# Performance work log

Hardware: AMD Instinct MI355X
Metric: run time of the kernel (lower is better)

The kernel has to match this reference:

```python
import jax, jax.numpy as jnp
import numpy as np

N, E, G = 150000, 600000, 5000
NI, EI, GF, H, C = 16, 8, 32, 64, 40


def setup_inputs() -> dict:
    key = jax.random.key(0)
    ks = jax.random.split(key, 20)
    s = lambda fan: 1.0 / np.sqrt(fan)
    return {
        "x": jax.random.normal(ks[0], (N, NI), jnp.float32),
        "edge_index": jax.random.randint(ks[1], (2, E), 0, N),
        "edge_attr": jax.random.normal(ks[2], (E, EI), jnp.float32),
        "batch": jnp.sort(jax.random.randint(ks[3], (N,), 0, G)),
        "pocket_features": jax.random.normal(ks[4], (G, GF), jnp.float32),
        # edge MLP: Linear(EI,H) -> ReLU -> Linear(H, H*NI)
        "W_e1": jax.random.normal(ks[5], (EI, H), jnp.float32) * s(EI),
        "b_e1": jnp.zeros((H,), jnp.float32),
        "W_e2": jax.random.normal(ks[6], (H, H * NI), jnp.float32) * s(H),
        "b_e2": jnp.zeros((H * NI,), jnp.float32),
        # NNConv root weight + bias
        "root": jax.random.normal(ks[7], (NI, H), jnp.float32) * s(NI),
        "conv_bias": jnp.zeros((H,), jnp.float32),
        # GlobalAttention gate Linear(H,1)
        "Wg": jax.random.normal(ks[8], (H, 1), jnp.float32) * s(H),
        "bg": jnp.zeros((1,), jnp.float32),
        # fc1: input is concat [h_node(H), global_ctx(H), pocket(GF)]
        "W_fc1": jax.random.normal(ks[9], (2 * H + GF, H), jnp.float32) * s(2 * H + GF),
        "b_fc1": jnp.zeros((H,), jnp.float32),
        "W_np": jax.random.normal(ks[10], (H, C), jnp.float32) * s(H),
        "b_np": jnp.zeros((C,), jnp.float32),
        "W_sp": jax.random.normal(ks[11], (H, 1), jnp.float32) * s(H),
        "b_sp": jnp.zeros((1,), jnp.float32),
    }


def reference(x, edge_index, edge_attr, batch, pocket_features,
              W_e1, b_e1, W_e2, b_e2, root, conv_bias, Wg, bg,
              W_fc1, b_fc1, W_np, b_np, W_sp, b_sp):
    n, ni = x.shape
    h = root.shape[1]
    g = pocket_features.shape[0]
    src, dst = edge_index[0], edge_index[1]

    # NNConv: edge MLP -> per-edge weight matrix [E, NI, H]
    eh = jax.nn.relu(edge_attr @ W_e1 + b_e1)
    We = (eh @ W_e2 + b_e2).reshape(-1, ni, h)
    msg = jnp.einsum('ei,eih->eh', x[src], We)          # per-edge matmul
    agg = jax.ops.segment_sum(msg, dst, num_segments=n)
    cnt = jax.ops.segment_sum(jnp.ones(msg.shape[0], x.dtype), dst, num_segments=n)
    agg = agg / jnp.maximum(cnt, 1.0)[:, None]          # aggr='mean'
    h_node = jax.nn.relu(agg + x @ root + conv_bias)    # [N, H]

    # GlobalAttention pooling: scatter-softmax over nodes per graph
    gate = (h_node @ Wg + bg).squeeze(-1)               # [N]
    m = jax.ops.segment_max(gate, batch, num_segments=g)
    e = jnp.exp(gate - m[batch])
    denom = jax.ops.segment_sum(e, batch, num_segments=g)
    attn = e / denom[batch]
    gctx = jax.ops.segment_sum(attn[:, None] * h_node, batch, num_segments=g)
    gc = gctx[batch]                                    # broadcast back [N, H]

    feat = jnp.concatenate([h_node, gc, pocket_features[batch]], axis=1)
    f = jax.nn.relu(feat @ W_fc1 + b_fc1)
    node_pred = jax.nn.log_softmax(f @ W_np + b_np, axis=-1)
    stop = jax.nn.sigmoid((gc @ W_sp + b_sp).squeeze(-1))
    return node_pred, stop
```

## Files before the change

kernel.cpp:

```cpp
#include <hip/hip_runtime.h>
#include <hip/hip_bf16.h>
#include <math.h>

#define NN 150000
#define EE 600000
#define GG 5000
#define NI 16
#define EI 8
#define GFD 32
#define HH 64
#define CC 40

#define W2SZ (68 * 1024)
#define FPAD 68
#define NBLK ((NN + 1023) / 1024)

typedef __attribute__((ext_vector_type(8))) short short8v;
typedef __attribute__((ext_vector_type(16))) float f32x16;
typedef __attribute__((ext_vector_type(2))) float f32x2;

__device__ __forceinline__ unsigned short f2bf(float f) {
    __hip_bfloat16 h = __float2bfloat16(f);
    return __builtin_bit_cast(unsigned short, h);
}
__device__ __forceinline__ float bf2f(unsigned short u) {
    return __uint_as_float(((unsigned)u) << 16);
}
__device__ __forceinline__ unsigned cvtpk(float lo, float hi) {
    unsigned r;
    asm("v_cvt_pk_bf16_f32 %0, %1, %2" : "=v"(r) : "v"(lo), "v"(hi));
    return r;
}
__device__ __forceinline__ f32x2 pkmul(f32x2 a, f32x2 b) {
    f32x2 p;
    asm("v_pk_mul_f32 %0, %1, %2" : "=v"(p) : "v"(a), "v"(b));
    return p;
}
__device__ __forceinline__ short8v zfrag(float eh, const f32x2 (&xs2)[4]) {
    f32x2 ehp; ehp[0] = eh; ehp[1] = eh;
    union { short8v v; unsigned u[4]; } A;
    #pragma unroll
    for (int q = 0; q < 4; ++q) {
        f32x2 p = pkmul(ehp, xs2[q]);
        A.u[q] = cvtpk(p[0], p[1]);
    }
    return A.v;
}
__device__ __forceinline__ short8v xfrag(const f32x2 (&xs2)[4]) {
    union { short8v v; unsigned u[4]; } A;
    #pragma unroll
    for (int q = 0; q < 4; ++q)
        A.u[q] = cvtpk(xs2[q][0], xs2[q][1]);
    return A.v;
}

__global__ void k0_prep(const float* __restrict__ W_e2, const float* __restrict__ b_e2,
                        const float* __restrict__ W_fc1, const float* __restrict__ W_np,
                        const float* __restrict__ W_e1,
                        unsigned short* __restrict__ W2c,
                        unsigned short* __restrict__ W1aT,
                        unsigned short* __restrict__ W_npT,
                        unsigned short* __restrict__ W1e,
                        int* __restrict__ cursor)
{
    int idx = blockIdx.x * 256 + threadIdx.x;
    if (idx < W2SZ) {
        int c = idx >> 10, rem = idx & 1023;
        int r = rem >> 4, kk = rem & 15;
        float v = 0.f;
        if (c < 64)       v = W_e2[c * 1024 + kk * 64 + r];
        else if (c == 64) v = b_e2[kk * 64 + r];
        W2c[idx] = f2bf(v);
    } else if (idx < W2SZ + 4096) {
        int i = idx - W2SZ;
        int h = i >> 6, k = i & 63;
        W1aT[i] = f2bf(W_fc1[k * 64 + h]);
    } else if (idx < W2SZ + 8192) {
        int i = idx - W2SZ - 4096;
        int c = i >> 6, h = i & 63;
        W_npT[i] = f2bf(c < CC ? W_np[h * CC + c] : 0.f);
    } else if (idx < W2SZ + 8704) {
        int i = idx - W2SZ - 8192;
        int col = i >> 3, q = i & 7;
        W1e[i] = f2bf(W_e1[q * 64 + col]);
    } else if (idx < W2SZ + 8704 + NN) {
        cursor[idx - W2SZ - 8704] = 0;
    }
}

__global__ void kE_local(const int* __restrict__ ei, int* __restrict__ cursor,
                         int* __restrict__ rank)
{
    int e = blockIdx.x * 256 + threadIdx.x;
    if (e < EE) rank[e] = atomicAdd(&cursor[ei[EE + e]], 1);
}

__global__ void kB_scan1(const int* __restrict__ cnt, int* __restrict__ base,
                         int* __restrict__ bsum)
{
    __shared__ int sS[256];
    int b = blockIdx.x, t = threadIdx.x;
    int i0 = b * 1024 + t * 4;
    int v0 = (i0 + 0 < NN) ? cnt[i0 + 0] : 0;
    int v1 = (i0 + 1 < NN) ? cnt[i0 + 1] : 0;
    int v2 = (i0 + 2 < NN) ? cnt[i0 + 2] : 0;
    int v3 = (i0 + 3 < NN) ? cnt[i0 + 3] : 0;
    int tot = v0 + v1 + v2 + v3;
    sS[t] = tot;
    __syncthreads();
    int acc = tot;
    for (int off = 1; off < 256; off <<= 1) {
        int xv = (t >= off) ? sS[t - off] : 0;
        __syncthreads();
        acc += xv;
        sS[t] = acc;
        __syncthreads();
    }
    int run = acc - tot;
    if (i0 + 0 < NN) base[i0 + 0] = run; run += v0;
    if (i0 + 1 < NN) base[i0 + 1] = run; run += v1;
    if (i0 + 2 < NN) base[i0 + 2] = run; run += v2;
    if (i0 + 3 < NN) base[i0 + 3] = run;
    if (t == 255) bsum[b] = acc;
}

__global__ void kC_scan2(int* __restrict__ bsum)
{
    __shared__ int sS[256];
    int t = threadIdx.x;
    int v = (t < NBLK) ? bsum[t] : 0;
    sS[t] = v;
    __syncthreads();
    int acc = v;
    for (int off = 1; off < 256; off <<= 1) {
        int xv = (t >= off) ? sS[t - off] : 0;
        __syncthreads();
        acc += xv;
        sS[t] = acc;
        __syncthreads();
    }
    if (t < NBLK) bsum[t] = acc - v;
}

__device__ __forceinline__ void mfma_step(
    const unsigned short (&sEHT)[65][256], int c, int pf,
    const unsigned short* __restrict__ Bq0, const unsigned short* __restrict__ Bq1,
    int mb, int mr, const f32x2 (&xs0)[4], const f32x2 (&xs1)[4],
    short8v& curb0, short8v& curb1,
    f32x16& acc00, f32x16& acc01, f32x16& acc10, f32x16& acc11)
{
    short8v n0 = *(const short8v*)(Bq0 + pf * 1024);
    short8v n1 = *(const short8v*)(Bq1 + pf * 1024);
    int cc = (c & 31) << 1;
    float eh0 = bf2f(sEHT[c][(mb + mr) ^ cc]);
    float eh1 = bf2f(sEHT[c][(mb + 32 + mr) ^ cc]);
    short8v a0 = zfrag(eh0, xs0);
    short8v a1 = zfrag(eh1, xs1);
    __builtin_amdgcn_s_setprio(1);
    acc00 = __builtin_amdgcn_mfma_f32_32x32x16_bf16(a0, curb0, acc00, 0, 0, 0);
    acc01 = __builtin_amdgcn_mfma_f32_32x32x16_bf16(a0, curb1, acc01, 0, 0, 0);
    acc10 = __builtin_amdgcn_mfma_f32_32x32x16_bf16(a1, curb0, acc10, 0, 0, 0);
    acc11 = __builtin_amdgcn_mfma_f32_32x32x16_bf16(a1, curb1, acc11, 0, 0, 0);
    __builtin_amdgcn_s_setprio(0);
    curb0 = n0; curb1 = n1;
}

template<bool TWOPHASE>
__global__ __launch_bounds__(256, 4) void k1_mfma(
    const float* __restrict__ x, const int* __restrict__ ei,
    const float* __restrict__ ea,
    const unsigned short* __restrict__ W1e, const float* __restrict__ b_e1,
    const unsigned short* __restrict__ W2c,
    const int* __restrict__ rank, const int* __restrict__ base,
    const int* __restrict__ bsum,
    unsigned* __restrict__ msg16, float* __restrict__ agg)
{
    __shared__ unsigned short sEHT[65][256];
    __shared__ int sIdx[256];

    const int t = threadIdx.x;
    const long long eb = (long long)blockIdx.x * 256;

    const int lane = t & 63;
    const int w = t >> 6;
    const int mr = lane & 31;
    const int half = lane >> 5;
    const int mb = w * 64;

    {
        long long ge = eb + t;
        if (ge < EE) {
            int d = ei[EE + ge];
            sIdx[t] = TWOPHASE ? (base[d] + bsum[d >> 10] + rank[ge]) : d;
        } else {
            sIdx[t] = -1;
        }
        sEHT[64][t] = (unsigned short)0x3F80;
    }

    {
        short8v bW0, bW1;
        if (half == 0) {
            bW0 = *(const short8v*)(W1e + (size_t)mr * 8);
            bW1 = *(const short8v*)(W1e + (size_t)(32 + mr) * 8);
        } else {
            #pragma unroll
            for (int q = 0; q < 8; ++q) { bW0[q] = 0; bW1[q] = 0; }
        }
        float bias0 = b_e1[mr];
        float bias1 = b_e1[32 + mr];
        #pragma unroll
        for (int m = 0; m < 2; ++m) {
            int e_loc = w * 64 + m * 32 + mr;
            long long ge = eb + e_loc;
            short8v a;
            if (half == 0 && ge < EE) {
                const float4* eap = (const float4*)(ea + ge * EI);
                float4 u0 = eap[0], u1 = eap[1];
                union { short8v v; unsigned u[4]; } A;
                A.u[0] = cvtpk(u0.x, u0.y); A.u[1] = cvtpk(u0.z, u0.w);
                A.u[2] = cvtpk(u1.x, u1.y); A.u[3] = cvtpk(u1.z, u1.w);
                a = A.v;
            } else {
                #pragma unroll
                for (int q = 0; q < 8; ++q) a[q] = 0;
            }
            #pragma unroll
            for (int n = 0; n < 2; ++n) {
                f32x16 c_;
                #pragma unroll
                for (int r = 0; r < 16; ++r) c_[r] = 0.f;
                c_ = __builtin_amdgcn_mfma_f32_32x32x16_bf16(a, n ? bW1 : bW0, c_, 0, 0, 0);
                int kcol = n * 32 + mr;
                float bias = n ? bias1 : bias0;
                #pragma unroll
                for (int r = 0; r < 16; r += 2) {
                    int row = (r & 3) + 8 * (r >> 2) + 4 * half;
                    int e0 = w * 64 + m * 32 + row;
                    float v0 = fmaxf(c_[r]     + bias, 0.f);
                    float v1 = fmaxf(c_[r + 1] + bias, 0.f);
                    *(unsigned*)&sEHT[kcol][e0 ^ (mr << 1)] = cvtpk(v0, v1);
                }
            }
        }
    }

    f32x2 xs0[4], xs1[4];
    {
        long long e0 = eb + mb + mr;
        long long e1 = eb + mb + 32 + mr;
        if (e0 < EE) {
            int s0 = ei[e0];
            const float4* xp = (const float4*)(x + (size_t)s0 * NI + half * 8);
            float4 u0 = xp[0], u1 = xp[1];
            xs0[0][0]=u0.x; xs0[0][1]=u0.y; xs0[1][0]=u0.z; xs0[1][1]=u0.w;
            xs0[2][0]=u1.x; xs0[2][1]=u1.y; xs0[3][0]=u1.z; xs0[3][1]=u1.w;
        } else {
            #pragma unroll
            for (int q = 0; q < 4; ++q) { xs0[q][0] = 0.f; xs0[q][1] = 0.f; }
        }
        if (e1 < EE) {
            int s1 = ei[e1];
            const float4* xp = (const float4*)(x + (size_t)s1 * NI + half * 8);
            float4 u0 = xp[0], u1 = xp[1];
            xs1[0][0]=u0.x; xs1[0][1]=u0.y; xs1[1][0]=u0.z; xs1[1][1]=u0.w;
            xs1[2][0]=u1.x; xs1[2][1]=u1.y; xs1[3][0]=u1.z; xs1[3][1]=u1.w;
        } else {
            #pragma unroll
            for (int q = 0; q < 4; ++q) { xs1[q][0] = 0.f; xs1[q][1] = 0.f; }
        }
    }
    __syncthreads();

    f32x16 acc00, acc01, acc10, acc11;
    #pragma unroll
    for (int r = 0; r < 16; ++r) { acc00[r] = 0.f; acc01[r] = 0.f; acc10[r] = 0.f; acc11[r] = 0.f; }

    const unsigned short* Bq0 = W2c + mr * 16 + half * 8;
    const unsigned short* Bq1 = Bq0 + 512;

    short8v bA0 = *(const short8v*)(Bq0);
    short8v bA1 = *(const short8v*)(Bq1);
    short8v bB0 = *(const short8v*)(Bq0 + 1024);
    short8v bB1 = *(const short8v*)(Bq1 + 1024);

    #pragma unroll 2
    for (int c = 0; c < 64; c += 2) {
        mfma_step(sEHT, c,     c + 2, Bq0, Bq1, mb, mr, xs0, xs1, bA0, bA1, acc00, acc01, acc10, acc11);
        mfma_step(sEHT, c + 1, c + 3, Bq0, Bq1, mb, mr, xs0, xs1, bB0, bB1, acc00, acc01, acc10, acc11);
    }
    {
        short8v a0 = xfrag(xs0);
        short8v a1 = xfrag(xs1);
        __builtin_amdgcn_s_setprio(1);
        acc00 = __builtin_amdgcn_mfma_f32_32x32x16_bf16(a0, bA0, acc00, 0, 0, 0);
        acc01 = __builtin_amdgcn_mfma_f32_32x32x16_bf16(a0, bA1, acc01, 0, 0, 0);
        acc10 = __builtin_amdgcn_mfma_f32_32x32x16_bf16(a1, bA0, acc10, 0, 0, 0);
        acc11 = __builtin_amdgcn_mfma_f32_32x32x16_bf16(a1, bA1, acc11, 0, 0, 0);
        __builtin_amdgcn_s_setprio(0);
    }

    #pragma unroll
    for (int r = 0; r < 16; ++r) {
        int row = (r & 3) + 8 * (r >> 2) + 4 * half;
        int i0 = sIdx[mb + row];
        int i1 = sIdx[mb + 32 + row];
        if (TWOPHASE) {
            if (i0 >= 0) msg16[(size_t)i0 * 32 + mr] = cvtpk(acc00[r], acc01[r]);
            if (i1 >= 0) msg16[(size_t)i1 * 32 + mr] = cvtpk(acc10[r], acc11[r]);
        } else {
            if (i0 >= 0) {
                atomicAdd(&agg[(size_t)i0 * 64 + mr],      acc00[r]);
                atomicAdd(&agg[(size_t)i0 * 64 + 32 + mr], acc01[r]);
            }
            if (i1 >= 0) {
                atomicAdd(&agg[(size_t)i1 * 64 + mr],      acc10[r]);
                atomicAdd(&agg[(size_t)i1 * 64 + 32 + mr], acc11[r]);
            }
        }
    }
}

__global__ __launch_bounds__(256) void k2_red(
    const unsigned* __restrict__ msg16, const int* __restrict__ base,
    const int* __restrict__ bsum,
    const float* __restrict__ x, const float* __restrict__ root,
    const float* __restrict__ conv_bias,
    unsigned short* __restrict__ hn16,
    const float* __restrict__ Wg, const float* __restrict__ bg,
    float* __restrict__ gate)
{
    __shared__ float sroot[16][64];
    int t = threadIdx.x;
    #pragma unroll
    for (int q = 0; q < 4; ++q) {
        int i = q * 256 + t;
        sroot[i >> 6][i & 63] = root[i];
    }
    __syncthreads();

    int n = blockIdx.x * 4 + (t >> 6);
    int l = t & 63;
    int mr = l & 31, so = l >> 5;
    int s = base[n] + bsum[n >> 10];
    int e = (n == NN - 1) ? EE : base[n + 1] + bsum[(n + 1) >> 10];

    float alo = 0.f, ahi = 0.f;
    for (int sl = s + so; sl < e; sl += 2) {
        unsigned u = msg16[(size_t)sl * 32 + mr];
        alo += __uint_as_float(u << 16);
        ahi += __uint_as_float(u & 0xFFFF0000u);
    }
    alo += __shfl_xor(alo, 32);
    ahi += __shfl_xor(ahi, 32);
    float acc = (l < 32) ? alo : ahi;

    float inv = 1.0f / fmaxf((float)(e - s), 1.0f);
    float v = acc * inv + conv_bias[l];
    float xv = (l < 16) ? x[(size_t)n * NI + l] : 0.f;
    #pragma unroll
    for (int i = 0; i < 16; ++i)
        v = fmaf(__shfl(xv, i), sroot[i][l], v);
    v = fmaxf(v, 0.f);
    hn16[(size_t)n * 64 + l] = f2bf(v);

    float gv = v * Wg[l];
    #pragma unroll
    for (int off = 32; off; off >>= 1) gv += __shfl_xor(gv, off);
    if (l == 0) gate[n] = gv + bg[0];
}

__global__ __launch_bounds__(256) void k2_node(
    const float* __restrict__ agg, const int* __restrict__ base,
    const int* __restrict__ bsum,
    const float* __restrict__ x, const float* __restrict__ root,
    const float* __restrict__ conv_bias,
    unsigned short* __restrict__ hn16,
    const float* __restrict__ Wg, const float* __restrict__ bg,
    float* __restrict__ gate)
{
    int t = threadIdx.x;
    int n = blockIdx.x * 4 + (t >> 6);
    int h = t & 63;
    int s = base[n] + bsum[n >> 10];
    int e = (n == NN - 1) ? EE : base[n + 1] + bsum[(n + 1) >> 10];
    float inv = 1.0f / fmaxf((float)(e - s), 1.0f);
    float v = agg[(size_t)n * 64 + h] * inv + conv_bias[h];
    const float* xp = x + (size_t)n * NI;
    #pragma unroll
    for (int i = 0; i < NI; ++i) v += xp[i] * root[i * 64 + h];
    v = fmaxf(v, 0.f);
    hn16[(size_t)n * 64 + h] = f2bf(v);
    float gv = v * Wg[h];
    #pragma unroll
    for (int off = 32; off; off >>= 1) gv += __shfl_xor(gv, off);
    if (h == 0) gate[n] = gv + bg[0];
}

__device__ __forceinline__ int lbound(const int* __restrict__ b, int v) {
    int lo = 0, hi = NN;
    while (lo < hi) { int mid = (lo + hi) >> 1; if (b[mid] < v) lo = mid + 1; else hi = mid; }
    return lo;
}

__global__ __launch_bounds__(64) void k3_pool(
    const float* __restrict__ gate, const int* __restrict__ batch,
    const unsigned short* __restrict__ hn16, const float* __restrict__ pocket,
    const float* __restrict__ W_fc1, const float* __restrict__ b_fc1,
    const float* __restrict__ W_sp, const float* __restrict__ b_sp,
    float* __restrict__ pg, float* __restrict__ sg)
{
    int g = blockIdx.x;
    int lane = threadIdx.x;
    int s = lbound(batch, g);
    int e = lbound(batch, g + 1);

    float gcv = 0.f;
    if (e > s) {
        float m = -INFINITY;
        for (int n = s + lane; n < e; n += 64) m = fmaxf(m, gate[n]);
        #pragma unroll
        for (int off = 32; off; off >>= 1) m = fmaxf(m, __shfl_xor(m, off));
        float acc = 0.f, den = 0.f;
        for (int n = s; n < e; ++n) {
            float ev = expf(gate[n] - m);
            den += ev;
            acc += ev * bf2f(hn16[(size_t)n * 64 + lane]);
        }
        gcv = acc / den;
    }

    float sv = gcv * W_sp[lane];
    #pragma unroll
    for (int off = 32; off; off >>= 1) sv += __shfl_xor(sv, off);
    if (lane == 0) sg[g] = 1.f / (1.f + expf(-(sv + b_sp[0])));

    float pk = (lane < GFD) ? pocket[(size_t)g * GFD + lane] : 0.f;
    float pgv = b_fc1[lane];
    #pragma unroll 8
    for (int kk = 0; kk < 64; ++kk)
        pgv = fmaf(__shfl(gcv, kk), W_fc1[(64 + kk) * 64 + lane], pgv);
    #pragma unroll 8
    for (int kk = 0; kk < 32; ++kk)
        pgv = fmaf(__shfl(pk, kk), W_fc1[(128 + kk) * 64 + lane], pgv);
    pg[(size_t)g * 64 + lane] = pgv;
}

__global__ __launch_bounds__(256, 4) void k4_mfma(
    const unsigned short* __restrict__ hn16, const int* __restrict__ batch,
    const float* __restrict__ pg, const float* __restrict__ sg,
    const unsigned short* __restrict__ W1aT, const unsigned short* __restrict__ W_npT,
    const float* __restrict__ b_np,
    float* __restrict__ out_np, float* __restrict__ out_stop)
{
    __shared__ __align__(16) float sF[4][32][FPAD];
    __shared__ int sB[128];

    const int t = threadIdx.x;
    const int wv = t >> 6, lane = t & 63;
    const int mr = lane & 31, half = lane >> 5;
    const int nb = blockIdx.x * 128;

    if (t < 128) {
        int n = nb + t;
        sB[t] = (n < NN) ? batch[n] : 0;
    }

    const int node = nb + wv * 32 + mr;

    f32x16 acc0, acc1;
    #pragma unroll
    for (int r = 0; r < 16; ++r) { acc0[r] = 0.f; acc1[r] = 0.f; }

    #pragma unroll
    for (int c = 0; c < 4; ++c) {
        short8v a;
        if (node < NN) {
            a = *(const short8v*)(hn16 + (size_t)node * 64 + c * 16 + half * 8);
        } else {
            #pragma unroll
            for (int q = 0; q < 8; ++q) a[q] = 0;
        }
        short8v b0 = *(const short8v*)(W1aT + (size_t)mr * 64        + c * 16 + half * 8);
        short8v b1 = *(const short8v*)(W1aT + (size_t)(mr + 32) * 64 + c * 16 + half * 8);
        acc0 = __builtin_amdgcn_mfma_f32_32x32x16_bf16(a, b0, acc0, 0, 0, 0);
        acc1 = __builtin_amdgcn_mfma_f32_32x32x16_bf16(a, b1, acc1, 0, 0, 0);
    }
    __syncthreads();

    #pragma unroll
    for (int r = 0; r < 16; ++r) {
        int row = (r & 3) + 8 * (r >> 2) + 4 * half;
        int g = sB[wv * 32 + row];
        float p0 = pg[(size_t)g * 64 + mr];
        float p1 = pg[(size_t)g * 64 + 32 + mr];
        sF[wv][row][mr]      = fmaxf(acc0[r] + p0, 0.f);
        sF[wv][row][32 + mr] = fmaxf(acc1[r] + p1, 0.f);
    }

    f32x16 acc2, acc3;
    #pragma unroll
    for (int r = 0; r < 16; ++r) { acc2[r] = 0.f; acc3[r] = 0.f; }

    #pragma unroll
    for (int c = 0; c < 4; ++c) {
        const float* fp = &sF[wv][mr][c * 16 + half * 8];
        float4 u0 = *(const float4*)(fp);
        float4 u1 = *(const float4*)(fp + 4);
        union { short8v v; unsigned u[4]; } A;
        A.u[0] = cvtpk(u0.x, u0.y); A.u[1] = cvtpk(u0.z, u0.w);
        A.u[2] = cvtpk(u1.x, u1.y); A.u[3] = cvtpk(u1.z, u1.w);
        short8v a = A.v;
        short8v b0 = *(const short8v*)(W_npT + (size_t)mr * 64        + c * 16 + half * 8);
        short8v b1 = *(const short8v*)(W_npT + (size_t)(mr + 32) * 64 + c * 16 + half * 8);
        acc2 = __builtin_amdgcn_mfma_f32_32x32x16_bf16(a, b0, acc2, 0, 0, 0);
        acc3 = __builtin_amdgcn_mfma_f32_32x32x16_bf16(a, b1, acc3, 0, 0, 0);
    }

    float bn1 = b_np[mr];
    float bn2 = (mr < 8) ? b_np[32 + mr] : 0.f;

    #pragma unroll
    for (int r = 0; r < 16; ++r) {
        int row = (r & 3) + 8 * (r >> 2) + 4 * half;
        int n = nb + wv * 32 + row;
        float v1 = acc2[r] + bn1;
        float v2 = acc3[r] + bn2;
        float m = (mr < 8) ? fmaxf(v1, v2) : v1;
        #pragma unroll
        for (int off = 16; off; off >>= 1) m = fmaxf(m, __shfl_xor(m, off));
        float s = expf(v1 - m) + ((mr < 8) ? expf(v2 - m) : 0.f);
        #pragma unroll
        for (int off = 16; off; off >>= 1) s += __shfl_xor(s, off);
        float ls = m + logf(s);
        if (n < NN) {
            out_np[(size_t)n * CC + mr] = v1 - ls;
            if (mr < 8) out_np[(size_t)n * CC + 32 + mr] = v2 - ls;
            if (mr == 0) out_stop[n] = sg[sB[wv * 32 + row]];
        }
    }
}

extern "C" void kernel_launch(void* const* d_in, const int* in_sizes, int n_in,
                              void* d_out, int out_size, void* d_ws, size_t ws_size,
                              hipStream_t stream)
{
    (void)in_sizes; (void)n_in; (void)out_size;
    const float* x        = (const float*)d_in[0];
    const int*   ei       = (const int*)d_in[1];
    const float* ea       = (const float*)d_in[2];
    const int*   batch    = (const int*)d_in[3];
    const float* pocket   = (const float*)d_in[4];
    const float* W_e1     = (const float*)d_in[5];
    const float* b_e1     = (const float*)d_in[6];
    const float* W_e2     = (const float*)d_in[7];
    const float* b_e2     = (const float*)d_in[8];
    const float* root     = (const float*)d_in[9];
    const float* conv_b   = (const float*)d_in[10];
    const float* Wg       = (const float*)d_in[11];
    const float* bg       = (const float*)d_in[12];
    const float* W_fc1    = (const float*)d_in[13];
    const float* b_fc1    = (const float*)d_in[14];
    const float* W_np     = (const float*)d_in[15];
    const float* b_np     = (const float*)d_in[16];
    const float* W_sp     = (const float*)d_in[17];
    const float* b_sp     = (const float*)d_in[18];

    char* wsb = (char*)d_ws;
    float* agg    = (float*)wsb;
    int*   base   = (int*)(agg + (size_t)NN * 64);
    int*   bsum   = base + NN + 4;
    int*   cursor = bsum + 256;
    int*   rank   = cursor + NN;
    float* gate   = (float*)(rank + EE);
    float* pg     = gate + NN;
    float* sg     = pg + (size_t)GG * 64;
    unsigned short* hn16  = (unsigned short*)(sg + GG);
    unsigned short* W2c   = hn16 + (size_t)NN * 64;
    unsigned short* W1aT  = W2c + W2SZ;
    unsigned short* W_npT = W1aT + 4096;
    unsigned short* W1e   = W_npT + 4096;
    size_t head = (size_t)((char*)(W1e + 512) - wsb);
    size_t msg_off = (head + 255) & ~(size_t)255;
    unsigned* msg16 = (unsigned*)(wsb + msg_off);
    size_t need = msg_off + (size_t)EE * 32 * sizeof(unsigned);
    const bool twophase = (ws_size >= need);

    k0_prep<<<(W2SZ + 8704 + NN + 255) / 256, 256, 0, stream>>>(
        W_e2, b_e2, W_fc1, W_np, W_e1, W2c, W1aT, W_npT, W1e, cursor);

    kE_local<<<(EE + 255) / 256, 256, 0, stream>>>(ei, cursor, rank);
    kB_scan1<<<NBLK, 256, 0, stream>>>(cursor, base, bsum);
    kC_scan2<<<1, 256, 0, stream>>>(bsum);

    if (twophase) {
        k1_mfma<true><<<(EE + 255) / 256, 256, 0, stream>>>(
            x, ei, ea, W1e, b_e1, W2c, rank, base, bsum, msg16, agg);
        k2_red<<<NN / 4, 256, 0, stream>>>(msg16, base, bsum, x, root, conv_b,
                                           hn16, Wg, bg, gate);
    } else {
        hipMemsetAsync(agg, 0, (size_t)NN * 64 * sizeof(float), stream);
        k1_mfma<false><<<(EE + 255) / 256, 256, 0, stream>>>(
            x, ei, ea, W1e, b_e1, W2c, rank, base, bsum, msg16, agg);
        k2_node<<<NN / 4, 256, 0, stream>>>(agg, base, bsum, x, root, conv_b,
                                            hn16, Wg, bg, gate);
    }

    k3_pool<<<GG, 64, 0, stream>>>(gate, batch, hn16, pocket, W_fc1, b_fc1, W_sp, b_sp, pg, sg);

    float* out_np   = (float*)d_out;
    float* out_stop = out_np + (size_t)NN * CC;
    k4_mfma<<<(NN + 127) / 128, 256, 0, stream>>>(hn16, batch, pg, sg, W1aT, W_npT, b_np,
                                                  out_np, out_stop);
}
```

Measured before the change: 259.9 us.

## Halve edges per block in edge MFMA kernel, row-major edge-hidden LDS, unroll reductions

```diff
diff --git a/kernel.cpp b/kernel.cpp
--- a/kernel.cpp
+++ b/kernel.cpp
@@ -12,10 +12,12 @@
 #define CC 40
 
 #define W2SZ (68 * 1024)
+#define EHS 72
 #define FPAD 68
 #define NBLK ((NN + 1023) / 1024)
 
 typedef __attribute__((ext_vector_type(8))) short short8v;
+typedef __attribute__((ext_vector_type(8))) unsigned short ushort8v;
 typedef __attribute__((ext_vector_type(16))) float f32x16;
 typedef __attribute__((ext_vector_type(2))) float f32x2;
 
@@ -142,31 +144,8 @@
     if (t < NBLK) bsum[t] = acc - v;
 }
 
-__device__ __forceinline__ void mfma_step(
-    const unsigned short (&sEHT)[65][256], int c, int pf,
-    const unsigned short* __restrict__ Bq0, const unsigned short* __restrict__ Bq1,
-    int mb, int mr, const f32x2 (&xs0)[4], const f32x2 (&xs1)[4],
-    short8v& curb0, short8v& curb1,
-    f32x16& acc00, f32x16& acc01, f32x16& acc10, f32x16& acc11)
-{
-    short8v n0 = *(const short8v*)(Bq0 + pf * 1024);
-    short8v n1 = *(const short8v*)(Bq1 + pf * 1024);
-    int cc = (c & 31) << 1;
-    float eh0 = bf2f(sEHT[c][(mb + mr) ^ cc]);
-    float eh1 = bf2f(sEHT[c][(mb + 32 + mr) ^ cc]);
-    short8v a0 = zfrag(eh0, xs0);
-    short8v a1 = zfrag(eh1, xs1);
-    __builtin_amdgcn_s_setprio(1);
-    acc00 = __builtin_amdgcn_mfma_f32_32x32x16_bf16(a0, curb0, acc00, 0, 0, 0);
-    acc01 = __builtin_amdgcn_mfma_f32_32x32x16_bf16(a0, curb1, acc01, 0, 0, 0);
-    acc10 = __builtin_amdgcn_mfma_f32_32x32x16_bf16(a1, curb0, acc10, 0, 0, 0);
-    acc11 = __builtin_amdgcn_mfma_f32_32x32x16_bf16(a1, curb1, acc11, 0, 0, 0);
-    __builtin_amdgcn_s_setprio(0);
-    curb0 = n0; curb1 = n1;
-}
-
 template<bool TWOPHASE>
-__global__ __launch_bounds__(256, 4) void k1_mfma(
+__global__ __launch_bounds__(256, 5) void k1_mfma(
     const float* __restrict__ x, const int* __restrict__ ei,
     const float* __restrict__ ea,
     const unsigned short* __restrict__ W1e, const float* __restrict__ b_e1,
@@ -175,19 +154,19 @@
     const int* __restrict__ bsum,
     unsigned* __restrict__ msg16, float* __restrict__ agg)
 {
-    __shared__ unsigned short sEHT[65][256];
-    __shared__ int sIdx[256];
+    __shared__ unsigned short sEHT2[128][EHS];
+    __shared__ int sIdx[128];
 
     const int t = threadIdx.x;
-    const long long eb = (long long)blockIdx.x * 256;
+    const long long eb = (long long)blockIdx.x * 128;
 
     const int lane = t & 63;
     const int w = t >> 6;
     const int mr = lane & 31;
     const int half = lane >> 5;
-    const int mb = w * 64;
-
-    {
+    const int mb2 = w * 32;
+
+    if (t < 128) {
         long long ge = eb + t;
         if (ge < EE) {
             int d = ei[EE + ge];
@@ -195,7 +174,6 @@
         } else {
             sIdx[t] = -1;
         }
-        sEHT[64][t] = (unsigned short)0x3F80;
     }
 
     {
@@ -209,72 +187,54 @@
         }
         float bias0 = b_e1[mr];
         float bias1 = b_e1[32 + mr];
+        long long ge = eb + mb2 + mr;
+        short8v a;
+        if (half == 0 && ge < EE) {
+            const float4* eap = (const float4*)(ea + ge * EI);
+            float4 u0 = eap[0], u1 = eap[1];
+            union { short8v v; unsigned u[4]; } A;
+            A.u[0] = cvtpk(u0.x, u0.y); A.u[1] = cvtpk(u0.z, u0.w);
+            A.u[2] = cvtpk(u1.x, u1.y); A.u[3] = cvtpk(u1.z, u1.w);
+            a = A.v;
+        } else {
+            #pragma unroll
+            for (int q = 0; q < 8; ++q) a[q] = 0;
+        }
         #pragma unroll
-        for (int m = 0; m < 2; ++m) {
-            int e_loc = w * 64 + m * 32 + mr;
-            long long ge = eb + e_loc;
-            short8v a;
-            if (half == 0 && ge < EE) {
-                const float4* eap = (const float4*)(ea + ge * EI);
-                float4 u0 = eap[0], u1 = eap[1];
-                union { short8v v; unsigned u[4]; } A;
-                A.u[0] = cvtpk(u0.x, u0.y); A.u[1] = cvtpk(u0.z, u0.w);
-                A.u[2] = cvtpk(u1.x, u1.y); A.u[3] = cvtpk(u1.z, u1.w);
-                a = A.v;
-            } else {
-                #pragma unroll
-                for (int q = 0; q < 8; ++q) a[q] = 0;
+        for (int n = 0; n < 2; ++n) {
+            f32x16 c_;
+            #pragma unroll
+            for (int r = 0; r < 16; ++r) c_[r] = 0.f;
+            c_ = __builtin_amdgcn_mfma_f32_32x32x16_bf16(a, n ? bW1 : bW0, c_, 0, 0, 0);
+            int kcol = n * 32 + mr;
+            float bias = n ? bias1 : bias0;
+            #pragma unroll
+            for (int r = 0; r < 16; ++r) {
+                int row = (r & 3) + 8 * (r >> 2) + 4 * half;
+                sEHT2[mb2 + row][kcol] = f2bf(fmaxf(c_[r] + bias, 0.f));
             }
-            #pragma unroll
-            for (int n = 0; n < 2; ++n) {
-                f32x16 c_;
-                #pragma unroll
-                for (int r = 0; r < 16; ++r) c_[r] = 0.f;
-                c_ = __builtin_amdgcn_mfma_f32_32x32x16_bf16(a, n ? bW1 : bW0, c_, 0, 0, 0);
-                int kcol = n * 32 + mr;
-                float bias = n ? bias1 : bias0;
-                #pragma unroll
-                for (int r = 0; r < 16; r += 2) {
-                    int row = (r & 3) + 8 * (r >> 2) + 4 * half;
-                    int e0 = w * 64 + m * 32 + row;
-                    float v0 = fmaxf(c_[r]     + bias, 0.f);
-                    float v1 = fmaxf(c_[r + 1] + bias, 0.f);
-                    *(unsigned*)&sEHT[kcol][e0 ^ (mr << 1)] = cvtpk(v0, v1);
-                }
-            }
-        }
-    }
-
-    f32x2 xs0[4], xs1[4];
+        }
+    }
+
+    f32x2 xs[4];
     {
-        long long e0 = eb + mb + mr;
-        long long e1 = eb + mb + 32 + mr;
-        if (e0 < EE) {
-            int s0 = ei[e0];
+        long long ge = eb + mb2 + mr;
+        if (ge < EE) {
+            int s0 = ei[ge];
             const float4* xp = (const float4*)(x + (size_t)s0 * NI + half * 8);
             float4 u0 = xp[0], u1 = xp[1];
-            xs0[0][0]=u0.x; xs0[0][1]=u0.y; xs0[1][0]=u0.z; xs0[1][1]=u0.w;
-            xs0[2][0]=u1.x; xs0[2][1]=u1.y; xs0[3][0]=u1.z; xs0[3][1]=u1.w;
+            xs[0][0]=u0.x; xs[0][1]=u0.y; xs[1][0]=u0.z; xs[1][1]=u0.w;
+            xs[2][0]=u1.x; xs[2][1]=u1.y; xs[3][0]=u1.z; xs[3][1]=u1.w;
         } else {
             #pragma unroll
-            for (int q = 0; q < 4; ++q) { xs0[q][0] = 0.f; xs0[q][1] = 0.f; }
-        }
-        if (e1 < EE) {
-            int s1 = ei[e1];
-            const float4* xp = (const float4*)(x + (size_t)s1 * NI + half * 8);
-            float4 u0 = xp[0], u1 = xp[1];
-            xs1[0][0]=u0.x; xs1[0][1]=u0.y; xs1[1][0]=u0.z; xs1[1][1]=u0.w;
-            xs1[2][0]=u1.x; xs1[2][1]=u1.y; xs1[3][0]=u1.z; xs1[3][1]=u1.w;
-        } else {
-            #pragma unroll
-            for (int q = 0; q < 4; ++q) { xs1[q][0] = 0.f; xs1[q][1] = 0.f; }
+            for (int q = 0; q < 4; ++q) { xs[q][0] = 0.f; xs[q][1] = 0.f; }
         }
     }
     __syncthreads();
 
-    f32x16 acc00, acc01, acc10, acc11;
-    #pragma unroll
-    for (int r = 0; r < 16; ++r) { acc00[r] = 0.f; acc01[r] = 0.f; acc10[r] = 0.f; acc11[r] = 0.f; }
+    f32x16 acc0, acc1;
+    #pragma unroll
+    for (int r = 0; r < 16; ++r) { acc0[r] = 0.f; acc1[r] = 0.f; }
 
     const unsigned short* Bq0 = W2c + mr * 16 + half * 8;
     const unsigned short* Bq1 = Bq0 + 512;
@@ -284,38 +244,56 @@
     short8v bB0 = *(const short8v*)(Bq0 + 1024);
     short8v bB1 = *(const short8v*)(Bq1 + 1024);
 
-    #pragma unroll 2
-    for (int c = 0; c < 64; c += 2) {
-        mfma_step(sEHT, c,     c + 2, Bq0, Bq1, mb, mr, xs0, xs1, bA0, bA1, acc00, acc01, acc10, acc11);
-        mfma_step(sEHT, c + 1, c + 3, Bq0, Bq1, mb, mr, xs0, xs1, bB0, bB1, acc00, acc01, acc10, acc11);
+    const unsigned short* ehp = &sEHT2[mb2 + mr][0];
+    ushort8v ehCur = *(const ushort8v*)(ehp);
+
+    #pragma unroll 1
+    for (int cb = 0; cb < 64; cb += 8) {
+        ushort8v ehNext = *(const ushort8v*)(ehp + cb + 8);
+        #pragma unroll
+        for (int j = 0; j < 8; j += 2) {
+            int c = cb + j;
+            {
+                short8v n0 = *(const short8v*)(Bq0 + (c + 2) * 1024);
+                short8v n1 = *(const short8v*)(Bq1 + (c + 2) * 1024);
+                short8v a = zfrag(bf2f(ehCur[j]), xs);
+                __builtin_amdgcn_s_setprio(1);
+                acc0 = __builtin_amdgcn_mfma_f32_32x32x16_bf16(a, bA0, acc0, 0, 0, 0);
+                acc1 = __builtin_amdgcn_mfma_f32_32x32x16_bf16(a, bA1, acc1, 0, 0, 0);
+                __builtin_amdgcn_s_setprio(0);
+                bA0 = n0; bA1 = n1;
+            }
+            {
+                short8v n0 = *(const short8v*)(Bq0 + (c + 3) * 1024);
+                short8v n1 = *(const short8v*)(Bq1 + (c + 3) * 1024);
+                short8v a = zfrag(bf2f(ehCur[j + 1]), xs);
+                __builtin_amdgcn_s_setprio(1);
+                acc0 = __builtin_amdgcn_mfma_f32_32x32x16_bf16(a, bB0, acc0, 0, 0, 0);
+                acc1 = __builtin_amdgcn_mfma_f32_32x32x16_bf16(a, bB1, acc1, 0, 0, 0);
+                __builtin_amdgcn_s_setprio(0);
+                bB0 = n0; bB1 = n1;
+            }
+        }
+        ehCur = ehNext;
     }
     {
-        short8v a0 = xfrag(xs0);
-        short8v a1 = xfrag(xs1);
+        short8v a = xfrag(xs);
         __builtin_amdgcn_s_setprio(1);
-        acc00 = __builtin_amdgcn_mfma_f32_32x32x16_bf16(a0, bA0, acc00, 0, 0, 0);
-        acc01 = __builtin_amdgcn_mfma_f32_32x32x16_bf16(a0, bA1, acc01, 0, 0, 0);
-        acc10 = __builtin_amdgcn_mfma_f32_32x32x16_bf16(a1, bA0, acc10, 0, 0, 0);
-        acc11 = __builtin_amdgcn_mfma_f32_32x32x16_bf16(a1, bA1, acc11, 0, 0, 0);
+        acc0 = __builtin_amdgcn_mfma_f32_32x32x16_bf16(a, bA0, acc0, 0, 0, 0);
+        acc1 = __builtin_amdgcn_mfma_f32_32x32x16_bf16(a, bA1, acc1, 0, 0, 0);
         __builtin_amdgcn_s_setprio(0);
     }
 
     #pragma unroll
     for (int r = 0; r < 16; ++r) {
         int row = (r & 3) + 8 * (r >> 2) + 4 * half;
-        int i0 = sIdx[mb + row];
-        int i1 = sIdx[mb + 32 + row];
+        int i0 = sIdx[mb2 + row];
         if (TWOPHASE) {
-            if (i0 >= 0) msg16[(size_t)i0 * 32 + mr] = cvtpk(acc00[r], acc01[r]);
-            if (i1 >= 0) msg16[(size_t)i1 * 32 + mr] = cvtpk(acc10[r], acc11[r]);
+            if (i0 >= 0) msg16[(size_t)i0 * 32 + mr] = cvtpk(acc0[r], acc1[r]);
         } else {
             if (i0 >= 0) {
-                atomicAdd(&agg[(size_t)i0 * 64 + mr],      acc00[r]);
-                atomicAdd(&agg[(size_t)i0 * 64 + 32 + mr], acc01[r]);
-            }
-            if (i1 >= 0) {
-                atomicAdd(&agg[(size_t)i1 * 64 + mr],      acc10[r]);
-                atomicAdd(&agg[(size_t)i1 * 64 + 32 + mr], acc11[r]);
+                atomicAdd(&agg[(size_t)i0 * 64 + mr],      acc0[r]);
+                atomicAdd(&agg[(size_t)i0 * 64 + 32 + mr], acc1[r]);
             }
         }
     }
@@ -346,7 +324,14 @@
     int e = (n == NN - 1) ? EE : base[n + 1] + bsum[(n + 1) >> 10];
 
     float alo = 0.f, ahi = 0.f;
-    for (int sl = s + so; sl < e; sl += 2) {
+    int sl = s + so;
+    for (; sl + 2 < e; sl += 4) {
+        unsigned u0 = msg16[(size_t)sl * 32 + mr];
+        unsigned u1 = msg16[(size_t)(sl + 2) * 32 + mr];
+        alo += __uint_as_float(u0 << 16) + __uint_as_float(u1 << 16);
+        ahi += __uint_as_float(u0 & 0xFFFF0000u) + __uint_as_float(u1 & 0xFFFF0000u);
+    }
+    if (sl < e) {
         unsigned u = msg16[(size_t)sl * 32 + mr];
         alo += __uint_as_float(u << 16);
         ahi += __uint_as_float(u & 0xFFFF0000u);
@@ -422,10 +407,20 @@
         #pragma unroll
         for (int off = 32; off; off >>= 1) m = fmaxf(m, __shfl_xor(m, off));
         float acc = 0.f, den = 0.f;
-        for (int n = s; n < e; ++n) {
+        int n = s;
+        for (; n + 2 <= e; n += 2) {
+            float e0 = expf(gate[n] - m);
+            float e1 = expf(gate[n + 1] - m);
+            float h0 = bf2f(hn16[(size_t)n * 64 + lane]);
+            float h1 = bf2f(hn16[(size_t)(n + 1) * 64 + lane]);
+            den += e0 + e1;
+            acc = fmaf(e0, h0, acc);
+            acc = fmaf(e1, h1, acc);
+        }
+        if (n < e) {
             float ev = expf(gate[n] - m);
             den += ev;
-            acc += ev * bf2f(hn16[(size_t)n * 64 + lane]);
+            acc = fmaf(ev, bf2f(hn16[(size_t)n * 64 + lane]), acc);
         }
         gcv = acc / den;
     }
@@ -594,13 +589,13 @@
     kC_scan2<<<1, 256, 0, stream>>>(bsum);
 
     if (twophase) {
-        k1_mfma<true><<<(EE + 255) / 256, 256, 0, stream>>>(
+        k1_mfma<true><<<(EE + 127) / 128, 256, 0, stream>>>(
             x, ei, ea, W1e, b_e1, W2c, rank, base, bsum, msg16, agg);
         k2_red<<<NN / 4, 256, 0, stream>>>(msg16, base, bsum, x, root, conv_b,
                                            hn16, Wg, bg, gate);
     } else {
         hipMemsetAsync(agg, 0, (size_t)NN * 64 * sizeof(float), stream);
-        k1_mfma<false><<<(EE + 255) / 256, 256, 0, stream>>>(
+        k1_mfma<false><<<(EE + 127) / 128, 256, 0, stream>>>(
             x, ei, ea, W1e, b_e1, W2c, rank, base, bsum, msg16, agg);
         k2_node<<<NN / 4, 256, 0, stream>>>(agg, base, bsum, x, root, conv_b,
                                             hn16, Wg, bg, gate);
```

Result: no change. 255.1 us (-1.8%).
